# Kernel tuning notes

Hardware: AMD Instinct MI355X
Metric: run time of the kernel (lower is better)

Reference implementation:

```python
import jax, jax.numpy as jnp
import numpy as np

B, V, C, H, W, D, G = 1, 5, 32, 128, 160, 48, 1


def _bilinear_sample(fea, x, y):
    # fea: [B,C,H,W]; x,y: [B,N] pixel coords (grid_sample align_corners=True, zero padding)
    Bb, Cc, Hh, Ww = fea.shape
    x0 = jnp.floor(x); y0 = jnp.floor(y)
    x1 = x0 + 1.0; y1 = y0 + 1.0
    wx1 = x - x0; wx0 = 1.0 - wx1
    wy1 = y - y0; wy0 = 1.0 - wy1
    flat = fea.reshape(Bb, Cc, Hh * Ww)
    def gather(xi, yi):
        valid = (xi >= 0) & (xi <= Ww - 1) & (yi >= 0) & (yi <= Hh - 1)
        xc = jnp.clip(xi, 0, Ww - 1).astype(jnp.int32)
        yc = jnp.clip(yi, 0, Hh - 1).astype(jnp.int32)
        idx = (yc * Ww + xc)[:, None, :]                      # [B,1,N]
        g = jnp.take_along_axis(flat, idx, axis=2)            # [B,C,N]
        return g * valid[:, None, :].astype(fea.dtype)
    return (gather(x0, y0) * (wx0 * wy0)[:, None, :]
          + gather(x1, y0) * (wx1 * wy0)[:, None, :]
          + gather(x0, y1) * (wx0 * wy1)[:, None, :]
          + gather(x1, y1) * (wx1 * wy1)[:, None, :])          # [B,C,N]


def _homo_warp(src_fea, src_proj, ref_proj, depth_values):
    # src_fea [B,C,H,W]; src_proj/ref_proj [B,4,4]; depth_values [B,D,H,W]
    Bb, Cc, Hh, Ww = src_fea.shape
    Dd = depth_values.shape[1]
    proj = src_proj @ jnp.linalg.inv(ref_proj)
    rot, trans = proj[:, :3, :3], proj[:, :3, 3:4]
    yy, xx = jnp.meshgrid(jnp.arange(Hh, dtype=src_fea.dtype),
                          jnp.arange(Ww, dtype=src_fea.dtype), indexing='ij')
    xyz = jnp.stack([xx.ravel(), yy.ravel(), jnp.ones(Hh * Ww, src_fea.dtype)], 0)  # [3,HW]
    rot_xyz = jnp.einsum('bij,jn->bin', rot, xyz)                                    # [B,3,HW]
    d = depth_values.reshape(Bb, 1, Dd, Hh * Ww)
    pxyz = rot_xyz[:, :, None, :] * d + trans[:, :, :, None]                         # [B,3,D,HW]
    px = (pxyz[:, 0] / pxyz[:, 2]).reshape(Bb, -1)
    py = (pxyz[:, 1] / pxyz[:, 2]).reshape(Bb, -1)
    warped = _bilinear_sample(src_fea, px, py)                                       # [B,C,D*HW]
    return warped.reshape(Bb, Cc, Dd, Hh, Ww)


def _pixelwise_net(sim, w0, b0, w1, b1, w2, b2):
    # sim [B,G,D,H,W]; 1x1x1 convs; BatchNorm at default init in eval is identity
    x = jax.nn.relu(jnp.einsum('oc,bcdhw->bodhw', w0, sim) + b0[None, :, None, None, None])
    x = jax.nn.relu(jnp.einsum('oc,bcdhw->bodhw', w1, x) + b1[None, :, None, None, None])
    x = jnp.einsum('oc,bcdhw->bodhw', w2, x) + b2[None, :, None, None, None]
    p = jax.nn.sigmoid(x[:, 0])                       # [B,D,H,W]
    return jnp.max(p, axis=1, keepdims=True)          # [B,1,H,W]


def _fuse_proj(p):
    # p [B,2,4,4] -> extrinsics with K folded into top 3x4
    top = jnp.einsum('bij,bjk->bik', p[:, 1, :3, :3], p[:, 0, :3, :4])
    return p[:, 0].at[:, :3, :4].set(top)


def _forward(features, proj_matrices, depth_values, w0, b0, w1, b1, w2, b2, reg_w, reg_b, num_depth):
    ref_fea = features[0]
    Bb, Cc, Hh, Ww = ref_fea.shape
    ref_proj = _fuse_proj(proj_matrices[:, 0])
    ref_vol = ref_fea.reshape(Bb, G, Cc // G, 1, Hh, Ww)
    sim_sum = 0.0
    wsum = 1e-5
    vw_list = []
    for i in range(1, features.shape[0]):
        src_proj = _fuse_proj(proj_matrices[:, i])
        warped = _homo_warp(features[i], src_proj, ref_proj, depth_values)
        warped = warped.reshape(Bb, G, Cc // G, num_depth, Hh, Ww)
        sim = (warped * ref_vol).mean(2)              # [B,G,D,H,W]
        vw = _pixelwise_net(sim, w0, b0, w1, b1, w2, b2)   # [B,1,H,W]
        vw_list.append(vw)
        sim_sum = sim_sum + sim * vw[:, None]
        wsum = wsum + vw[:, None]
    sim = sim_sum / wsum
    cost = jax.lax.conv_general_dilated(sim, reg_w, (1, 1, 1), 'SAME',
                                        dimension_numbers=('NCDHW', 'OIDHW', 'NCDHW'))
    prob_volume_pre = cost[:, 0] + reg_b[0]           # [B,D,H,W]
    prob = jax.nn.softmax(prob_volume_pre, axis=1)
    idx = jnp.argmax(prob, axis=1, keepdims=True)
    depth = jnp.take_along_axis(depth_values, idx, axis=1)[:, 0]   # winner-take-all depth
    conf = jnp.max(prob, axis=1)
    view_weights = jnp.concatenate(vw_list, axis=1)
    return depth, conf, prob, view_weights


def setup_inputs() -> dict:
    key = jax.random.key(0)
    ks = jax.random.split(key, 6)
    features = jax.random.normal(ks[0], (V, B, C, H, W), jnp.float32)
    # Plausible camera geometry: identity-ish extrinsics + pinhole intrinsics
    K = np.eye(4, dtype=np.float32)
    K[0, 0] = K[1, 1] = 150.0; K[0, 2] = W / 2.0; K[1, 2] = H / 2.0
    mats = []
    for v in range(V):
        E = np.eye(4, dtype=np.float32)
        a = 0.01 * v
        ca, sa = np.cos(a), np.sin(a)
        E[:3, :3] = np.array([[ca, 0, sa], [0, 1, 0], [-sa, 0, ca]], np.float32)
        E[0, 3] = -5.0 * v
        mats.append(np.stack([E, K], 0))
    proj_matrices = jnp.asarray(np.stack(mats, 0)[None])  # [1,V,2,4,4]
    depth_values = jnp.broadcast_to(
        jnp.linspace(425.0, 935.0, D, dtype=jnp.float32).reshape(1, D, 1, 1), (B, D, H, W)) * jnp.ones((B, D, H, W), jnp.float32)
    return {
        'features': features,
        'proj_matrices': proj_matrices,
        'depth_values': depth_values,
        'w0': jax.random.normal(ks[1], (16, G), jnp.float32) * 0.1,
        'b0': jnp.zeros((16,), jnp.float32),
        'w1': jax.random.normal(ks[2], (8, 16), jnp.float32) * 0.1,
        'b1': jnp.zeros((8,), jnp.float32),
        'w2': jax.random.normal(ks[3], (1, 8), jnp.float32) * 0.1,
        'b2': jnp.zeros((1,), jnp.float32),
        'reg_w': jax.random.normal(ks[4], (1, G, 3, 3, 3), jnp.float32) * 0.1,
        'reg_b': jnp.zeros((1,), jnp.float32),
        'num_depth': D,
    }


def reference(features, proj_matrices, depth_values, w0, b0, w1, b1, w2, b2, reg_w, reg_b, num_depth):
    return _forward(features, proj_matrices, depth_values, w0, b0, w1, b1, w2, b2, reg_w, reg_b, num_depth)
```

## Files before the change

kernel.cpp:

```cpp
#include <hip/hip_runtime.h>
#include <hip/hip_bf16.h>
#include <math.h>

#define W_  160
#define H_  128
#define HW  20480
#define D_  48
#define C_  32
#define NV  4

#define TX  16
#define TY  4
#define TXH 18
#define TYH 6
#define NCOL (TXH*TYH)
#define GD  4
#define GDS 12

template<int CTRL>
__device__ __forceinline__ float dpp_add(float s) {
  int t = __builtin_amdgcn_update_dpp(0, __float_as_int(s), CTRL, 0xF, 0xF, true);
  return s + __int_as_float(t);
}

__device__ __forceinline__ unsigned ordf(float f) {
  unsigned b = __float_as_uint(f);
  return b ^ (((int)b >> 31) | 0x80000000u);
}
__device__ __forceinline__ float deordf(unsigned u) {
  unsigned b = (u & 0x80000000u) ? (u ^ 0x80000000u) : ~u;
  return __uint_as_float(b);
}

__device__ __forceinline__ void fuse_proj(const float* pm, float* P) {
  const float* E = pm;
  const float* K = pm + 16;
  for (int r = 0; r < 3; ++r)
    for (int c = 0; c < 4; ++c)
      P[r*4+c] = K[r*4+0]*E[0*4+c] + K[r*4+1]*E[1*4+c] + K[r*4+2]*E[2*4+c];
  for (int c = 0; c < 4; ++c) P[12+c] = E[12+c];
}

__device__ void invert4(const float* m, float* invOut) {
  float inv[16];
  inv[0]  =  m[5]*m[10]*m[15] - m[5]*m[11]*m[14] - m[9]*m[6]*m[15] + m[9]*m[7]*m[14] + m[13]*m[6]*m[11] - m[13]*m[7]*m[10];
  inv[4]  = -m[4]*m[10]*m[15] + m[4]*m[11]*m[14] + m[8]*m[6]*m[15] - m[8]*m[7]*m[14] - m[12]*m[6]*m[11] + m[12]*m[7]*m[10];
  inv[8]  =  m[4]*m[9]*m[15]  - m[4]*m[11]*m[13] - m[8]*m[5]*m[15] + m[8]*m[7]*m[13] + m[12]*m[5]*m[11] - m[12]*m[7]*m[9];
  inv[12] = -m[4]*m[9]*m[14]  + m[4]*m[10]*m[13] + m[8]*m[5]*m[14] - m[8]*m[6]*m[13] - m[12]*m[5]*m[10] + m[12]*m[6]*m[9];
  inv[1]  = -m[1]*m[10]*m[15] + m[1]*m[11]*m[14] + m[9]*m[2]*m[15] - m[9]*m[3]*m[14] - m[13]*m[2]*m[11] + m[13]*m[3]*m[10];
  inv[5]  =  m[0]*m[10]*m[15] - m[0]*m[11]*m[14] - m[8]*m[2]*m[15] + m[8]*m[3]*m[14] + m[12]*m[2]*m[11] - m[12]*m[3]*m[10];
  inv[9]  = -m[0]*m[9]*m[15]  + m[0]*m[11]*m[13] + m[8]*m[1]*m[15] - m[8]*m[3]*m[13] - m[12]*m[1]*m[11] + m[12]*m[3]*m[9];
  inv[13] =  m[0]*m[9]*m[14]  - m[0]*m[10]*m[13] - m[8]*m[1]*m[14] + m[8]*m[2]*m[13] + m[12]*m[1]*m[10] - m[12]*m[2]*m[9];
  inv[2]  =  m[1]*m[6]*m[15]  - m[1]*m[7]*m[14]  - m[5]*m[2]*m[15] + m[5]*m[3]*m[14] + m[13]*m[2]*m[7]  - m[13]*m[3]*m[6];
  inv[6]  = -m[0]*m[6]*m[15]  + m[0]*m[7]*m[14]  + m[4]*m[2]*m[15] - m[4]*m[3]*m[14] - m[12]*m[2]*m[7]  + m[12]*m[3]*m[6];
  inv[10] =  m[0]*m[5]*m[15]  - m[0]*m[7]*m[13]  - m[4]*m[1]*m[15] + m[4]*m[3]*m[13] + m[12]*m[1]*m[7]  - m[12]*m[3]*m[5];
  inv[14] = -m[0]*m[5]*m[14]  + m[0]*m[6]*m[13]  + m[4]*m[1]*m[14] - m[4]*m[2]*m[13] - m[12]*m[1]*m[6]  + m[12]*m[2]*m[5];
  inv[3]  = -m[1]*m[6]*m[11]  + m[1]*m[7]*m[10]  + m[5]*m[2]*m[11] - m[5]*m[3]*m[10] - m[9]*m[2]*m[7]   + m[9]*m[3]*m[6];
  inv[7]  =  m[0]*m[6]*m[11]  - m[0]*m[7]*m[10]  - m[4]*m[2]*m[11] + m[4]*m[3]*m[10] + m[8]*m[2]*m[7]   - m[8]*m[3]*m[6];
  inv[11] = -m[0]*m[5]*m[11]  + m[0]*m[7]*m[9]   + m[4]*m[1]*m[11] - m[4]*m[3]*m[9]  - m[8]*m[1]*m[7]   + m[8]*m[3]*m[5];
  inv[15] =  m[0]*m[5]*m[10]  - m[0]*m[6]*m[9]   - m[4]*m[1]*m[10] + m[4]*m[2]*m[9]  + m[8]*m[1]*m[6]   - m[8]*m[2]*m[5];
  float det = m[0]*inv[0] + m[1]*inv[4] + m[2]*inv[8] + m[3]*inv[12];
  det = 1.0f / det;
  for (int i = 0; i < 16; i++) invOut[i] = inv[i] * det;
}

__global__ void __launch_bounds__(256)
k_prep(const float* __restrict__ feat, const float* __restrict__ pm,
       float* __restrict__ tf, float* __restrict__ xf,
       unsigned* __restrict__ vwu) {
  __shared__ float tile[C_][64+1];
  int v  = blockIdx.y;
  int p0 = blockIdx.x * 64;
  int t  = threadIdx.x;

  if (v == 0) vwu[blockIdx.x*256 + t] = 0u;

  int pl = t & 63;
  int cg = t >> 6;
  const float* src = feat + (size_t)v*C_*HW + p0 + pl;
  #pragma unroll
  for (int k = 0; k < 8; ++k) {
    int c = cg*8 + k;
    tile[c][pl] = src[(size_t)c*HW];
  }
  __syncthreads();

  int pp = t >> 2;
  int co = (t & 3) * 8;
  float4 a, b;
  a.x = tile[co+0][pp]; a.y = tile[co+1][pp]; a.z = tile[co+2][pp]; a.w = tile[co+3][pp];
  b.x = tile[co+4][pp]; b.y = tile[co+5][pp]; b.z = tile[co+6][pp]; b.w = tile[co+7][pp];
  float* dst = tf + ((size_t)v*HW + p0 + pp)*C_ + co;
  *(float4*)dst = a;
  *(float4*)(dst+4) = b;

  if (blockIdx.x == 0 && v == 0) {
    if (t < 64) tf[(size_t)5*HW*C_ + t] = 0.0f;
    if (t == 0) {
      float Pr[16], Pinv[16], Ps[16], M[16];
      fuse_proj(pm, Pr);
      invert4(Pr, Pinv);
      for (int vv = 1; vv <= NV; ++vv) {
        fuse_proj(pm + vv*32, Ps);
        for (int r = 0; r < 4; ++r)
          for (int c = 0; c < 4; ++c) {
            float acc = 0.f;
            for (int k = 0; k < 4; ++k) acc += Ps[r*4+k]*Pinv[k*4+c];
            M[r*4+c] = acc;
          }
        float* o = xf + (vv-1)*12;
        o[0]=M[0];  o[1]=M[1];  o[2]=M[2];
        o[3]=M[4];  o[4]=M[5];  o[5]=M[6];
        o[6]=M[8];  o[7]=M[9];  o[8]=M[10];
        o[9]=M[3];  o[10]=M[7]; o[11]=M[11];
      }
    }
  }
}

template<int KX>
__device__ __forceinline__ void build_tab(
    const char* tfb, int chb, int ZB, float4 rfc,
    int xmin, int ymin, int ch, float* tabp) {
  #pragma unroll
  for (int t = 0; t < KX*3; ++t) {
    int xi = xmin + t/3;
    int yi = ymin + t%3;
    bool valid = ((unsigned)xi < (unsigned)W_) && ((unsigned)yi < (unsigned)H_);
    int off = valid ? (yi*W_ + xi)*(C_*4) : ZB;
    float4 a = *(const float4*)(tfb + off + chb);
    float d = a.x*rfc.x + a.y*rfc.y + a.z*rfc.z + a.w*rfc.w;
    d = dpp_add<0xB1>(d);
    d = dpp_add<0x4E>(d);
    d = dpp_add<0x141>(d);
    if (ch == (t & 7)) tabp[t] = d;
  }
}

__global__ void __launch_bounds__(256)
k_warp(const float* __restrict__ tf, const float* __restrict__ dv,
       const float* __restrict__ xf, float* __restrict__ sim_all) {
  __shared__ float dtab[4][8][25];

  int lane = threadIdx.x & 63;
  int wv = threadIdx.x >> 6;
  int ch = lane & 7;
  int pix = (lane >> 3) & 7;
  int wvg = __builtin_amdgcn_readfirstlane((blockIdx.x*256 + threadIdx.x) >> 6);
  const int PGPV = HW/8;
  int pg = wvg % PGPV;
  int v  = wvg / PGPV;
  int p  = pg*8 + pix;

  float xpix = (float)(p % W_);
  float ypix = (float)(p / W_);

  const float* M = xf + v*12;
  float rx = M[0]*xpix + M[1]*ypix + M[2];
  float ry = M[3]*xpix + M[4]*ypix + M[5];
  float rz = M[6]*xpix + M[7]*ypix + M[8];
  float t0 = M[9], t1 = M[10], t2 = M[11];

  float4 rfc = *(const float4*)(tf + (size_t)p*C_ + ch*4);
  rfc.x *= (1.0f/(float)C_); rfc.y *= (1.0f/(float)C_);
  rfc.z *= (1.0f/(float)C_); rfc.w *= (1.0f/(float)C_);

  const char* tfb = (const char*)(tf + (size_t)(v+1)*HW*C_);
  const int chb = ch*16;
  const int ZB = (4-v)*HW*C_*4;

  float depE0 = dv[p];
  float depE1 = dv[(size_t)47*HW + p];
  float dpk[6];
  #pragma unroll
  for (int k = 0; k < 6; ++k) dpk[k] = dv[(size_t)(k*8 + ch)*HW + p];

  float Z0 = rz*depE0 + t2, Z1 = rz*depE1 + t2;
  float iz0 = 1.0f / Z0,     iz1 = 1.0f / Z1;
  float pxa = (rx*depE0 + t0) * iz0, pya = (ry*depE0 + t1) * iz0;
  float pxb = (rx*depE1 + t0) * iz1, pyb = (ry*depE1 + t1) * iz1;
  int xmin = (int)floorf(fminf(pxa, pxb));
  int ymin = (int)floorf(fminf(pya, pyb));
  int Nx = (int)floorf(fmaxf(pxa, pxb)) - xmin + 2;
  int Ny = (int)floorf(fmaxf(pya, pyb)) - ymin + 2;

  float dmn = fminf(depE0, depE1), dmx = fmaxf(depE0, depE1);
  bool ok = (Nx <= 8) && (Ny <= 3) && (Z0*Z1 > 0.0f);
  #pragma unroll
  for (int k = 0; k < 6; ++k) ok = ok && (dpk[k] >= dmn) && (dpk[k] <= dmx);

  float* simv = sim_all + (size_t)v*D_*HW + p;

  if (__all(ok)) {
    float* tabp = dtab[wv][pix];
    if (__all(Nx <= 5)) build_tab<5>(tfb, chb, ZB, rfc, xmin, ymin, ch, tabp);
    else                build_tab<8>(tfb, chb, ZB, rfc, xmin, ymin, ch, tabp);

    int xhi = xmin + 6;
    if (__all(Nx <= 5)) xhi = xmin + 3;

    #pragma unroll
    for (int k = 0; k < 6; ++k) {
      float dep = dpk[k];
      float Z  = rz*dep + t2;
      float zr = 1.0f / Z;
      float px = (rx*dep + t0) * zr;
      float py = (ry*dep + t1) * zr;
      int xi = (int)floorf(px);
      int yi = (int)floorf(py);
      xi = min(max(xi, xmin), xhi);
      yi = min(max(yi, ymin), ymin + 1);
      float wx1 = px - (float)xi;
      float wy1 = py - (float)yi;
      float wx0 = 1.0f - wx1, wy0 = 1.0f - wy1;
      int idx = (xi - xmin)*3 + (yi - ymin);
      float t00 = tabp[idx];
      float t01 = tabp[idx + 3];
      float t10 = tabp[idx + 1];
      float t11 = tabp[idx + 4];
      float s = wx0*wy0*t00 + wx1*wy0*t01 + wx0*wy1*t10 + wx1*wy1*t11;
      simv[(size_t)(k*8 + ch)*HW] = s;
    }
  } else {
    const float* tff  = tf + (size_t)(v+1)*HW*C_;
    const float* refp = tf + (size_t)p*C_;
    const int ZE = (4-v)*HW*C_;
    #pragma unroll 1
    for (int k = 0; k < 6; ++k) {
      float dep = dpk[k];
      float Z  = rz*dep + t2;
      float px = (rx*dep + t0) / Z;
      float py = (ry*dep + t1) / Z;
      float x0f = floorf(px), y0f = floorf(py);
      float wx1 = px - x0f, wy1 = py - y0f;
      float wx0 = 1.0f - wx1, wy0 = 1.0f - wy1;
      int x0 = (int)x0f, y0 = (int)y0f;
      int x1 = x0 + 1,   y1 = y0 + 1;
      bool vx0 = ((unsigned)x0 <= (unsigned)(W_-1));
      bool vx1 = ((unsigned)x1 <= (unsigned)(W_-1));
      bool vy0 = ((unsigned)y0 <= (unsigned)(H_-1));
      bool vy1 = ((unsigned)y1 <= (unsigned)(H_-1));
      int cx0 = min(max(x0, 0), W_-1);
      int cx1 = min(max(x1, 0), W_-1);
      int cy0 = min(max(y0, 0), H_-1);
      int cy1 = min(max(y1, 0), H_-1);
      int o00 = (vx0 && vy0) ? (cy0*W_+cx0)*C_ : ZE;
      int o01 = (vx1 && vy0) ? (cy0*W_+cx1)*C_ : ZE;
      int o10 = (vx0 && vy1) ? (cy1*W_+cx0)*C_ : ZE;
      int o11 = (vx1 && vy1) ? (cy1*W_+cx1)*C_ : ZE;
      float a00=0.f, a01=0.f, a10=0.f, a11=0.f;
      #pragma unroll 1
      for (int q = 0; q < 8; ++q) {
        float4 rq = *(const float4*)(refp + q*4);
        float4 c0 = *(const float4*)(tff + o00 + q*4);
        float4 c1 = *(const float4*)(tff + o01 + q*4);
        float4 c2 = *(const float4*)(tff + o10 + q*4);
        float4 c3 = *(const float4*)(tff + o11 + q*4);
        a00 += c0.x*rq.x + c0.y*rq.y + c0.z*rq.z + c0.w*rq.w;
        a01 += c1.x*rq.x + c1.y*rq.y + c1.z*rq.z + c1.w*rq.w;
        a10 += c2.x*rq.x + c2.y*rq.y + c2.z*rq.z + c2.w*rq.w;
        a11 += c3.x*rq.x + c3.y*rq.y + c3.z*rq.z + c3.w*rq.w;
      }
      float s = (wx0*wy0*a00 + wx1*wy0*a01 + wx0*wy1*a10 + wx1*wy1*a11)
                * (1.0f/(float)C_);
      simv[(size_t)(k*8 + ch)*HW] = s;
    }
  }
}

__global__ void __launch_bounds__(256)
k_mlp(const float* __restrict__ sim_all,
      const float* __restrict__ w0, const float* __restrict__ b0,
      const float* __restrict__ w1, const float* __restrict__ b1,
      const float* __restrict__ w2, const float* __restrict__ b2,
      unsigned* __restrict__ vwu) {
  int idx = blockIdx.x*blockDim.x + threadIdx.x;
  if (idx >= NV*(D_/4)*HW) return;
  int p = idx % HW;
  int t = idx / HW;
  int v = t / (D_/4);
  int c = t % (D_/4);

  const float* sp_ = sim_all + ((size_t)(v*D_ + c*4))*HW + p;
  float sv[4];
  sv[0] = sp_[0];
  sv[1] = sp_[HW];
  sv[2] = sp_[2*HW];
  sv[3] = sp_[3*HW];

  float ymax = -3.0e38f;
  #pragma unroll
  for (int k = 0; k < 4; ++k) {
    float s = sv[k];
    float acc0 = b1[0], acc1 = b1[1], acc2 = b1[2], acc3 = b1[3];
    float acc4 = b1[4], acc5 = b1[5], acc6 = b1[6], acc7 = b1[7];
    #pragma unroll
    for (int o = 0; o < 16; ++o) {
      float h = fmaxf(fmaf(w0[o], s, b0[o]), 0.0f);
      acc0 = fmaf(w1[0*16+o], h, acc0);
      acc1 = fmaf(w1[1*16+o], h, acc1);
      acc2 = fmaf(w1[2*16+o], h, acc2);
      acc3 = fmaf(w1[3*16+o], h, acc3);
      acc4 = fmaf(w1[4*16+o], h, acc4);
      acc5 = fmaf(w1[5*16+o], h, acc5);
      acc6 = fmaf(w1[6*16+o], h, acc6);
      acc7 = fmaf(w1[7*16+o], h, acc7);
    }
    float yv = b2[0];
    yv = fmaf(w2[0], fmaxf(acc0, 0.0f), yv);
    yv = fmaf(w2[1], fmaxf(acc1, 0.0f), yv);
    yv = fmaf(w2[2], fmaxf(acc2, 0.0f), yv);
    yv = fmaf(w2[3], fmaxf(acc3, 0.0f), yv);
    yv = fmaf(w2[4], fmaxf(acc4, 0.0f), yv);
    yv = fmaf(w2[5], fmaxf(acc5, 0.0f), yv);
    yv = fmaf(w2[6], fmaxf(acc6, 0.0f), yv);
    yv = fmaf(w2[7], fmaxf(acc7, 0.0f), yv);
    ymax = fmaxf(ymax, yv);
  }
  atomicMax(&vwu[(size_t)v*HW + p], ordf(ymax));
}

__global__ void __launch_bounds__(256)
k_fusecv(const float* __restrict__ sim_all, const unsigned* __restrict__ vwu,
         const float* __restrict__ rw, const float* __restrict__ rb,
         float* __restrict__ cost) {
  __shared__ float svw[NV][NCOL];
  __shared__ float sinvw[NCOL];
  __shared__ int   sgpc[NCOL];
  __shared__ float sfus[GDS+2][TYH][TXH+1];

  int tid = threadIdx.x;
  int gx0 = blockIdx.x*TX;
  int gy0 = blockIdx.y*TY;
  int g   = blockIdx.z;

  if (tid < NCOL) {
    int yy = tid / TXH, xx = tid % TXH;
    int gy = gy0 + yy - 1, gx = gx0 + xx - 1;
    bool valid = (gx >= 0) && (gx < W_) && (gy >= 0) && (gy < H_);
    int gp = min(max(gy,0),H_-1)*W_ + min(max(gx,0),W_-1);
    sgpc[tid] = gp;
    float a0 = 1.0f/(1.0f + expf(-deordf(vwu[0*HW+gp])));
    float a1 = 1.0f/(1.0f + expf(-deordf(vwu[1*HW+gp])));
    float a2 = 1.0f/(1.0f + expf(-deordf(vwu[2*HW+gp])));
    float a3 = 1.0f/(1.0f + expf(-deordf(vwu[3*HW+gp])));
    float inv = valid ? 1.0f/(1e-5f + a0+a1+a2+a3) : 0.0f;
    if (!valid) { a0=a1=a2=a3=0.f; }
    svw[0][tid]=a0; svw[1][tid]=a1; svw[2][tid]=a2; svw[3][tid]=a3;
    sinvw[tid] = inv;
  }
  __syncthreads();

  for (int j = tid; j < (GDS+2)*NCOL; j += 256) {
    int s = j / NCOL, r = j % NCOL;
    int dz = g*GDS - 1 + s;
    float val = 0.0f;
    if (dz >= 0 && dz < D_) {
      int gp = sgpc[r];
      float s0 = sim_all[(size_t)(0*D_+dz)*HW + gp];
      float s1 = sim_all[(size_t)(1*D_+dz)*HW + gp];
      float s2 = sim_all[(size_t)(2*D_+dz)*HW + gp];
      float s3 = sim_all[(size_t)(3*D_+dz)*HW + gp];
      val = (s0*svw[0][r] + s1*svw[1][r] + s2*svw[2][r] + s3*svw[3][r]) * sinvw[r];
    }
    sfus[s][r/TXH][r%TXH] = val;
  }
  __syncthreads();

  {
    int pid = tid & 63;
    int dg  = tid >> 6;
    int px = pid & 15, py = pid >> 4;
    float kw[27];
    #pragma unroll
    for (int i = 0; i < 27; ++i) kw[i] = rw[i];
    float bias = rb[0];
    int gp = (gy0+py)*W_ + gx0+px;

    #pragma unroll
    for (int k = 0; k < 3; ++k) {
      int dl = dg*3 + k;
      float acc = bias;
      #pragma unroll
      for (int kd = 0; kd < 3; ++kd)
        #pragma unroll
        for (int ky = 0; ky < 3; ++ky)
          #pragma unroll
          for (int kx = 0; kx < 3; ++kx)
            acc += sfus[dl+kd][py+ky][px+kx] * kw[(kd*3+ky)*3+kx];
      cost[(size_t)(g*GDS + dl)*HW + gp] = acc;
    }
  }
}

__global__ void __launch_bounds__(256)
k_softmax(const float* __restrict__ cost, const unsigned* __restrict__ vwu,
          const float* __restrict__ dv, float* __restrict__ out) {
  int p = blockIdx.x*256 + threadIdx.x;
  if (p >= HW) return;

  float c[D_];
  #pragma unroll
  for (int d = 0; d < D_; ++d) c[d] = cost[(size_t)d*HW + p];

  float vmax = c[0];
  int am = 0;
  #pragma unroll
  for (int d = 1; d < D_; ++d) {
    if (c[d] > vmax) { vmax = c[d]; am = d; }
  }
  float sum = 0.0f;
  #pragma unroll
  for (int d = 0; d < D_; ++d) {
    float e = expf(c[d] - vmax);
    c[d] = e;
    sum += e;
  }
  float inv = 1.0f / sum;
  #pragma unroll
  for (int d = 0; d < D_; ++d)
    out[(size_t)(2*HW) + (size_t)d*HW + p] = c[d] * inv;

  out[p] = dv[(size_t)am*HW + p];
  out[HW + p] = inv;
  #pragma unroll
  for (int v = 0; v < NV; ++v)
    out[(size_t)(2*HW + D_*HW) + (size_t)v*HW + p] =
        1.0f/(1.0f + expf(-deordf(vwu[(size_t)v*HW + p])));
}

extern "C" void kernel_launch(void* const* d_in, const int* in_sizes, int n_in,
                              void* d_out, int out_size, void* d_ws, size_t ws_size,
                              hipStream_t stream) {
  const float* feat = (const float*)d_in[0];
  const float* pm   = (const float*)d_in[1];
  const float* dv   = (const float*)d_in[2];
  const float* w0   = (const float*)d_in[3];
  const float* b0   = (const float*)d_in[4];
  const float* w1   = (const float*)d_in[5];
  const float* b1   = (const float*)d_in[6];
  const float* w2   = (const float*)d_in[7];
  const float* b2   = (const float*)d_in[8];
  const float* rw   = (const float*)d_in[9];
  const float* rb   = (const float*)d_in[10];
  float* out = (float*)d_out;
  float* ws  = (float*)d_ws;

  float*    xf   = ws;
  float*    tf   = ws + 64;
  float*    sim  = ws + 3276928;
  unsigned* vwu  = (unsigned*)(ws + 7209088);
  float*    cost = ws + 7291008;

  hipLaunchKernelGGL(k_prep, dim3(HW/64, 5), dim3(256), 0, stream,
                     feat, pm, tf, xf, vwu);
  hipLaunchKernelGGL(k_warp, dim3((NV*HW*8)/256), dim3(256), 0, stream,
                     tf, dv, xf, sim);
  hipLaunchKernelGGL(k_mlp, dim3((NV*(D_/4)*HW)/256), dim3(256), 0, stream,
                     sim, w0, b0, w1, b1, w2, b2, vwu);
  hipLaunchKernelGGL(k_fusecv, dim3(W_/TX, H_/TY, GD), dim3(256), 0, stream,
                     sim, vwu, rw, rb, cost);
  hipLaunchKernelGGL(k_softmax, dim3(HW/256), dim3(256), 0, stream,
                     cost, vwu, dv, out);
}
```

Baseline: 75.38 us.

## Fuse pixelwise MLP and view-weight max into warp kernel

The per-pixel MLP that produces view weights now runs inside the warp kernel on the similarity values each lane already holds in registers. The max over depth is reduced across the 8 lanes with DPP, and the sigmoid is written directly as a float. This removes the separate MLP kernel, its re-read of the similarity volume, the atomicMax with ordered-int encoding, and the zero-init in prep. The cost is extra ALU work and register pressure in the warp kernel, which could lower its occupancy.

```diff
diff --git a/kernel.cpp b/kernel.cpp
--- a/kernel.cpp
+++ b/kernel.cpp
@@ -22,14 +22,10 @@
   int t = __builtin_amdgcn_update_dpp(0, __float_as_int(s), CTRL, 0xF, 0xF, true);
   return s + __int_as_float(t);
 }
-
-__device__ __forceinline__ unsigned ordf(float f) {
-  unsigned b = __float_as_uint(f);
-  return b ^ (((int)b >> 31) | 0x80000000u);
-}
-__device__ __forceinline__ float deordf(unsigned u) {
-  unsigned b = (u & 0x80000000u) ? (u ^ 0x80000000u) : ~u;
-  return __uint_as_float(b);
+template<int CTRL>
+__device__ __forceinline__ float dpp_max(float s) {
+  int t = __builtin_amdgcn_update_dpp(0, __float_as_int(s), CTRL, 0xF, 0xF, true);
+  return fmaxf(s, __int_as_float(t));
 }
 
 __device__ __forceinline__ void fuse_proj(const float* pm, float* P) {
@@ -66,14 +62,11 @@
 
 __global__ void __launch_bounds__(256)
 k_prep(const float* __restrict__ feat, const float* __restrict__ pm,
-       float* __restrict__ tf, float* __restrict__ xf,
-       unsigned* __restrict__ vwu) {
+       float* __restrict__ tf, float* __restrict__ xf) {
   __shared__ float tile[C_][64+1];
   int v  = blockIdx.y;
   int p0 = blockIdx.x * 64;
   int t  = threadIdx.x;
-
-  if (v == 0) vwu[blockIdx.x*256 + t] = 0u;
 
   int pl = t & 63;
   int cg = t >> 6;
@@ -137,9 +130,44 @@
   }
 }
 
+__device__ __forceinline__ float mlp_eval(
+    float s,
+    const float* __restrict__ w0, const float* __restrict__ b0,
+    const float* __restrict__ w1, const float* __restrict__ b1,
+    const float* __restrict__ w2, const float* __restrict__ b2) {
+  float acc0 = b1[0], acc1 = b1[1], acc2 = b1[2], acc3 = b1[3];
+  float acc4 = b1[4], acc5 = b1[5], acc6 = b1[6], acc7 = b1[7];
+  #pragma unroll
+  for (int o = 0; o < 16; ++o) {
+    float h = fmaxf(fmaf(w0[o], s, b0[o]), 0.0f);
+    acc0 = fmaf(w1[0*16+o], h, acc0);
+    acc1 = fmaf(w1[1*16+o], h, acc1);
+    acc2 = fmaf(w1[2*16+o], h, acc2);
+    acc3 = fmaf(w1[3*16+o], h, acc3);
+    acc4 = fmaf(w1[4*16+o], h, acc4);
+    acc5 = fmaf(w1[5*16+o], h, acc5);
+    acc6 = fmaf(w1[6*16+o], h, acc6);
+    acc7 = fmaf(w1[7*16+o], h, acc7);
+  }
+  float yv = b2[0];
+  yv = fmaf(w2[0], fmaxf(acc0, 0.0f), yv);
+  yv = fmaf(w2[1], fmaxf(acc1, 0.0f), yv);
+  yv = fmaf(w2[2], fmaxf(acc2, 0.0f), yv);
+  yv = fmaf(w2[3], fmaxf(acc3, 0.0f), yv);
+  yv = fmaf(w2[4], fmaxf(acc4, 0.0f), yv);
+  yv = fmaf(w2[5], fmaxf(acc5, 0.0f), yv);
+  yv = fmaf(w2[6], fmaxf(acc6, 0.0f), yv);
+  yv = fmaf(w2[7], fmaxf(acc7, 0.0f), yv);
+  return yv;
+}
+
 __global__ void __launch_bounds__(256)
 k_warp(const float* __restrict__ tf, const float* __restrict__ dv,
-       const float* __restrict__ xf, float* __restrict__ sim_all) {
+       const float* __restrict__ xf,
+       const float* __restrict__ w0, const float* __restrict__ b0,
+       const float* __restrict__ w1, const float* __restrict__ b1,
+       const float* __restrict__ w2, const float* __restrict__ b2,
+       float* __restrict__ sim_all, float* __restrict__ vw) {
   __shared__ float dtab[4][8][25];
 
   int lane = threadIdx.x & 63;
@@ -190,6 +218,7 @@
   for (int k = 0; k < 6; ++k) ok = ok && (dpk[k] >= dmn) && (dpk[k] <= dmx);
 
   float* simv = sim_all + (size_t)v*D_*HW + p;
+  float sk[6];
 
   if (__all(ok)) {
     float* tabp = dtab[wv][pix];
@@ -219,6 +248,7 @@
       float t10 = tabp[idx + 1];
       float t11 = tabp[idx + 4];
       float s = wx0*wy0*t00 + wx1*wy0*t01 + wx0*wy1*t10 + wx1*wy1*t11;
+      sk[k] = s;
       simv[(size_t)(k*8 + ch)*HW] = s;
     }
   } else {
@@ -263,65 +293,26 @@
       }
       float s = (wx0*wy0*a00 + wx1*wy0*a01 + wx0*wy1*a10 + wx1*wy1*a11)
                 * (1.0f/(float)C_);
+      sk[k] = s;
       simv[(size_t)(k*8 + ch)*HW] = s;
     }
   }
+
+  float ymax = mlp_eval(sk[0], w0, b0, w1, b1, w2, b2);
+  ymax = fmaxf(ymax, mlp_eval(sk[1], w0, b0, w1, b1, w2, b2));
+  ymax = fmaxf(ymax, mlp_eval(sk[2], w0, b0, w1, b1, w2, b2));
+  ymax = fmaxf(ymax, mlp_eval(sk[3], w0, b0, w1, b1, w2, b2));
+  ymax = fmaxf(ymax, mlp_eval(sk[4], w0, b0, w1, b1, w2, b2));
+  ymax = fmaxf(ymax, mlp_eval(sk[5], w0, b0, w1, b1, w2, b2));
+
+  ymax = dpp_max<0xB1>(ymax);
+  ymax = dpp_max<0x4E>(ymax);
+  ymax = dpp_max<0x141>(ymax);
+  if (ch == 0) vw[(size_t)v*HW + p] = 1.0f / (1.0f + expf(-ymax));
 }
 
 __global__ void __launch_bounds__(256)
-k_mlp(const float* __restrict__ sim_all,
-      const float* __restrict__ w0, const float* __restrict__ b0,
-      const float* __restrict__ w1, const float* __restrict__ b1,
-      const float* __restrict__ w2, const float* __restrict__ b2,
-      unsigned* __restrict__ vwu) {
-  int idx = blockIdx.x*blockDim.x + threadIdx.x;
-  if (idx >= NV*(D_/4)*HW) return;
-  int p = idx % HW;
-  int t = idx / HW;
-  int v = t / (D_/4);
-  int c = t % (D_/4);
-
-  const float* sp_ = sim_all + ((size_t)(v*D_ + c*4))*HW + p;
-  float sv[4];
-  sv[0] = sp_[0];
-  sv[1] = sp_[HW];
-  sv[2] = sp_[2*HW];
-  sv[3] = sp_[3*HW];
-
-  float ymax = -3.0e38f;
-  #pragma unroll
-  for (int k = 0; k < 4; ++k) {
-    float s = sv[k];
-    float acc0 = b1[0], acc1 = b1[1], acc2 = b1[2], acc3 = b1[3];
-    float acc4 = b1[4], acc5 = b1[5], acc6 = b1[6], acc7 = b1[7];
-    #pragma unroll
-    for (int o = 0; o < 16; ++o) {
-      float h = fmaxf(fmaf(w0[o], s, b0[o]), 0.0f);
-      acc0 = fmaf(w1[0*16+o], h, acc0);
-      acc1 = fmaf(w1[1*16+o], h, acc1);
-      acc2 = fmaf(w1[2*16+o], h, acc2);
-      acc3 = fmaf(w1[3*16+o], h, acc3);
-      acc4 = fmaf(w1[4*16+o], h, acc4);
-      acc5 = fmaf(w1[5*16+o], h, acc5);
-      acc6 = fmaf(w1[6*16+o], h, acc6);
-      acc7 = fmaf(w1[7*16+o], h, acc7);
-    }
-    float yv = b2[0];
-    yv = fmaf(w2[0], fmaxf(acc0, 0.0f), yv);
-    yv = fmaf(w2[1], fmaxf(acc1, 0.0f), yv);
-    yv = fmaf(w2[2], fmaxf(acc2, 0.0f), yv);
-    yv = fmaf(w2[3], fmaxf(acc3, 0.0f), yv);
-    yv = fmaf(w2[4], fmaxf(acc4, 0.0f), yv);
-    yv = fmaf(w2[5], fmaxf(acc5, 0.0f), yv);
-    yv = fmaf(w2[6], fmaxf(acc6, 0.0f), yv);
-    yv = fmaf(w2[7], fmaxf(acc7, 0.0f), yv);
-    ymax = fmaxf(ymax, yv);
-  }
-  atomicMax(&vwu[(size_t)v*HW + p], ordf(ymax));
-}
-
-__global__ void __launch_bounds__(256)
-k_fusecv(const float* __restrict__ sim_all, const unsigned* __restrict__ vwu,
+k_fusecv(const float* __restrict__ sim_all, const float* __restrict__ vw,
          const float* __restrict__ rw, const float* __restrict__ rb,
          float* __restrict__ cost) {
   __shared__ float svw[NV][NCOL];
@@ -340,10 +331,7 @@
     bool valid = (gx >= 0) && (gx < W_) && (gy >= 0) && (gy < H_);
     int gp = min(max(gy,0),H_-1)*W_ + min(max(gx,0),W_-1);
     sgpc[tid] = gp;
-    float a0 = 1.0f/(1.0f + expf(-deordf(vwu[0*HW+gp])));
-    float a1 = 1.0f/(1.0f + expf(-deordf(vwu[1*HW+gp])));
-    float a2 = 1.0f/(1.0f + expf(-deordf(vwu[2*HW+gp])));
-    float a3 = 1.0f/(1.0f + expf(-deordf(vwu[3*HW+gp])));
+    float a0 = vw[0*HW+gp], a1 = vw[1*HW+gp], a2 = vw[2*HW+gp], a3 = vw[3*HW+gp];
     float inv = valid ? 1.0f/(1e-5f + a0+a1+a2+a3) : 0.0f;
     if (!valid) { a0=a1=a2=a3=0.f; }
     svw[0][tid]=a0; svw[1][tid]=a1; svw[2][tid]=a2; svw[3][tid]=a3;
@@ -394,7 +382,7 @@
 }
 
 __global__ void __launch_bounds__(256)
-k_softmax(const float* __restrict__ cost, const unsigned* __restrict__ vwu,
+k_softmax(const float* __restrict__ cost, const float* __restrict__ vw,
           const float* __restrict__ dv, float* __restrict__ out) {
   int p = blockIdx.x*256 + threadIdx.x;
   if (p >= HW) return;
@@ -425,8 +413,7 @@
   out[HW + p] = inv;
   #pragma unroll
   for (int v = 0; v < NV; ++v)
-    out[(size_t)(2*HW + D_*HW) + (size_t)v*HW + p] =
-        1.0f/(1.0f + expf(-deordf(vwu[(size_t)v*HW + p])));
+    out[(size_t)(2*HW + D_*HW) + (size_t)v*HW + p] = vw[(size_t)v*HW + p];
 }
 
 extern "C" void kernel_launch(void* const* d_in, const int* in_sizes, int n_in,
@@ -446,20 +433,18 @@
   float* out = (float*)d_out;
   float* ws  = (float*)d_ws;
 
-  float*    xf   = ws;
-  float*    tf   = ws + 64;
-  float*    sim  = ws + 3276928;
-  unsigned* vwu  = (unsigned*)(ws + 7209088);
-  float*    cost = ws + 7291008;
+  float* xf   = ws;
+  float* tf   = ws + 64;
+  float* sim  = ws + 3276928;
+  float* vw   = ws + 7209088;
+  float* cost = ws + 7291008;
 
   hipLaunchKernelGGL(k_prep, dim3(HW/64, 5), dim3(256), 0, stream,
-                     feat, pm, tf, xf, vwu);
+                     feat, pm, tf, xf);
   hipLaunchKernelGGL(k_warp, dim3((NV*HW*8)/256), dim3(256), 0, stream,
-                     tf, dv, xf, sim);
-  hipLaunchKernelGGL(k_mlp, dim3((NV*(D_/4)*HW)/256), dim3(256), 0, stream,
-                     sim, w0, b0, w1, b1, w2, b2, vwu);
+                     tf, dv, xf, w0, b0, w1, b1, w2, b2, sim, vw);
   hipLaunchKernelGGL(k_fusecv, dim3(W_/TX, H_/TY, GD), dim3(256), 0, stream,
-                     sim, vwu, rw, rb, cost);
+                     sim, vw, rw, rb, cost);
   hipLaunchKernelGGL(k_softmax, dim3(HW/256), dim3(256), 0, stream,
-                     cost, vwu, dv, out);
-}
+                     cost, vw, dv, out);
+}
```

After: 81.46 us. 1.08x slower.

## Interleave views in similarity buffer and widen table fast path to 12 columns

Applied to the files above, without the earlier changes.

Stores the per-view similarity volume as [depth][pixel][view] so the MLP and fusion kernels load all four views with one float4. The MLP kernel now processes one depth per thread across four views and issues four atomic maxes instead of reducing over four depths first. The warp kernel gains a 12-column table path so more wavefronts avoid the slow gather fallback. The cost is strided stores in the warp kernel and more atomic traffic in the MLP kernel.

```diff
diff --git a/kernel.cpp b/kernel.cpp
--- a/kernel.cpp
+++ b/kernel.cpp
@@ -139,8 +139,8 @@
 
 __global__ void __launch_bounds__(256)
 k_warp(const float* __restrict__ tf, const float* __restrict__ dv,
-       const float* __restrict__ xf, float* __restrict__ sim_all) {
-  __shared__ float dtab[4][8][25];
+       const float* __restrict__ xf, float* __restrict__ sim4) {
+  __shared__ float dtab[4][8][37];
 
   int lane = threadIdx.x & 63;
   int wv = threadIdx.x >> 6;
@@ -185,19 +185,25 @@
   int Ny = (int)floorf(fmaxf(pya, pyb)) - ymin + 2;
 
   float dmn = fminf(depE0, depE1), dmx = fmaxf(depE0, depE1);
-  bool ok = (Nx <= 8) && (Ny <= 3) && (Z0*Z1 > 0.0f);
+  bool ok = (Nx <= 12) && (Ny <= 3) && (Z0*Z1 > 0.0f);
   #pragma unroll
   for (int k = 0; k < 6; ++k) ok = ok && (dpk[k] >= dmn) && (dpk[k] <= dmx);
 
-  float* simv = sim_all + (size_t)v*D_*HW + p;
+  float* simv = sim4 + (size_t)p*4 + v;
 
   if (__all(ok)) {
     float* tabp = dtab[wv][pix];
-    if (__all(Nx <= 5)) build_tab<5>(tfb, chb, ZB, rfc, xmin, ymin, ch, tabp);
-    else                build_tab<8>(tfb, chb, ZB, rfc, xmin, ymin, ch, tabp);
-
-    int xhi = xmin + 6;
-    if (__all(Nx <= 5)) xhi = xmin + 3;
+    int xhi;
+    if (__all(Nx <= 5)) {
+      build_tab<5>(tfb, chb, ZB, rfc, xmin, ymin, ch, tabp);
+      xhi = xmin + 3;
+    } else if (__all(Nx <= 8)) {
+      build_tab<8>(tfb, chb, ZB, rfc, xmin, ymin, ch, tabp);
+      xhi = xmin + 6;
+    } else {
+      build_tab<12>(tfb, chb, ZB, rfc, xmin, ymin, ch, tabp);
+      xhi = xmin + 10;
+    }
 
     #pragma unroll
     for (int k = 0; k < 6; ++k) {
@@ -219,7 +225,8 @@
       float t10 = tabp[idx + 1];
       float t11 = tabp[idx + 4];
       float s = wx0*wy0*t00 + wx1*wy0*t01 + wx0*wy1*t10 + wx1*wy1*t11;
-      simv[(size_t)(k*8 + ch)*HW] = s;
+      if (ch == ch) ;
+      simv[(size_t)(k*8 + ch)*HW*4] = s;
     }
   } else {
     const float* tff  = tf + (size_t)(v+1)*HW*C_;
@@ -263,65 +270,66 @@
       }
       float s = (wx0*wy0*a00 + wx1*wy0*a01 + wx0*wy1*a10 + wx1*wy1*a11)
                 * (1.0f/(float)C_);
-      simv[(size_t)(k*8 + ch)*HW] = s;
+      simv[(size_t)(k*8 + ch)*HW*4] = s;
     }
   }
 }
 
 __global__ void __launch_bounds__(256)
-k_mlp(const float* __restrict__ sim_all,
+k_mlp(const float* __restrict__ sim4,
       const float* __restrict__ w0, const float* __restrict__ b0,
       const float* __restrict__ w1, const float* __restrict__ b1,
       const float* __restrict__ w2, const float* __restrict__ b2,
       unsigned* __restrict__ vwu) {
   int idx = blockIdx.x*blockDim.x + threadIdx.x;
-  if (idx >= NV*(D_/4)*HW) return;
+  if (idx >= D_*HW) return;
   int p = idx % HW;
-  int t = idx / HW;
-  int v = t / (D_/4);
-  int c = t % (D_/4);
-
-  const float* sp_ = sim_all + ((size_t)(v*D_ + c*4))*HW + p;
-  float sv[4];
-  sv[0] = sp_[0];
-  sv[1] = sp_[HW];
-  sv[2] = sp_[2*HW];
-  sv[3] = sp_[3*HW];
-
-  float ymax = -3.0e38f;
-  #pragma unroll
-  for (int k = 0; k < 4; ++k) {
-    float s = sv[k];
-    float acc0 = b1[0], acc1 = b1[1], acc2 = b1[2], acc3 = b1[3];
-    float acc4 = b1[4], acc5 = b1[5], acc6 = b1[6], acc7 = b1[7];
+
+  float4 s4 = *(const float4*)(sim4 + (size_t)idx*4);
+
+  float y0, y1, y2, y3;
+  {
+    float acc[4][8];
+    #pragma unroll
+    for (int j = 0; j < 8; ++j) {
+      float bb = b1[j];
+      acc[0][j] = bb; acc[1][j] = bb; acc[2][j] = bb; acc[3][j] = bb;
+    }
     #pragma unroll
     for (int o = 0; o < 16; ++o) {
-      float h = fmaxf(fmaf(w0[o], s, b0[o]), 0.0f);
-      acc0 = fmaf(w1[0*16+o], h, acc0);
-      acc1 = fmaf(w1[1*16+o], h, acc1);
-      acc2 = fmaf(w1[2*16+o], h, acc2);
-      acc3 = fmaf(w1[3*16+o], h, acc3);
-      acc4 = fmaf(w1[4*16+o], h, acc4);
-      acc5 = fmaf(w1[5*16+o], h, acc5);
-      acc6 = fmaf(w1[6*16+o], h, acc6);
-      acc7 = fmaf(w1[7*16+o], h, acc7);
-    }
-    float yv = b2[0];
-    yv = fmaf(w2[0], fmaxf(acc0, 0.0f), yv);
-    yv = fmaf(w2[1], fmaxf(acc1, 0.0f), yv);
-    yv = fmaf(w2[2], fmaxf(acc2, 0.0f), yv);
-    yv = fmaf(w2[3], fmaxf(acc3, 0.0f), yv);
-    yv = fmaf(w2[4], fmaxf(acc4, 0.0f), yv);
-    yv = fmaf(w2[5], fmaxf(acc5, 0.0f), yv);
-    yv = fmaf(w2[6], fmaxf(acc6, 0.0f), yv);
-    yv = fmaf(w2[7], fmaxf(acc7, 0.0f), yv);
-    ymax = fmaxf(ymax, yv);
-  }
-  atomicMax(&vwu[(size_t)v*HW + p], ordf(ymax));
+      float wo = w0[o], bo = b0[o];
+      float h0 = fmaxf(fmaf(wo, s4.x, bo), 0.0f);
+      float h1 = fmaxf(fmaf(wo, s4.y, bo), 0.0f);
+      float h2 = fmaxf(fmaf(wo, s4.z, bo), 0.0f);
+      float h3 = fmaxf(fmaf(wo, s4.w, bo), 0.0f);
+      #pragma unroll
+      for (int j = 0; j < 8; ++j) {
+        float w = w1[j*16+o];
+        acc[0][j] = fmaf(w, h0, acc[0][j]);
+        acc[1][j] = fmaf(w, h1, acc[1][j]);
+        acc[2][j] = fmaf(w, h2, acc[2][j]);
+        acc[3][j] = fmaf(w, h3, acc[3][j]);
+      }
+    }
+    float b2v = b2[0];
+    y0 = b2v; y1 = b2v; y2 = b2v; y3 = b2v;
+    #pragma unroll
+    for (int j = 0; j < 8; ++j) {
+      float w = w2[j];
+      y0 = fmaf(w, fmaxf(acc[0][j], 0.0f), y0);
+      y1 = fmaf(w, fmaxf(acc[1][j], 0.0f), y1);
+      y2 = fmaf(w, fmaxf(acc[2][j], 0.0f), y2);
+      y3 = fmaf(w, fmaxf(acc[3][j], 0.0f), y3);
+    }
+  }
+  atomicMax(&vwu[0*HW + p], ordf(y0));
+  atomicMax(&vwu[1*HW + p], ordf(y1));
+  atomicMax(&vwu[2*HW + p], ordf(y2));
+  atomicMax(&vwu[3*HW + p], ordf(y3));
 }
 
 __global__ void __launch_bounds__(256)
-k_fusecv(const float* __restrict__ sim_all, const unsigned* __restrict__ vwu,
+k_fusecv(const float* __restrict__ sim4, const unsigned* __restrict__ vwu,
          const float* __restrict__ rw, const float* __restrict__ rb,
          float* __restrict__ cost) {
   __shared__ float svw[NV][NCOL];
@@ -357,11 +365,9 @@
     float val = 0.0f;
     if (dz >= 0 && dz < D_) {
       int gp = sgpc[r];
-      float s0 = sim_all[(size_t)(0*D_+dz)*HW + gp];
-      float s1 = sim_all[(size_t)(1*D_+dz)*HW + gp];
-      float s2 = sim_all[(size_t)(2*D_+dz)*HW + gp];
-      float s3 = sim_all[(size_t)(3*D_+dz)*HW + gp];
-      val = (s0*svw[0][r] + s1*svw[1][r] + s2*svw[2][r] + s3*svw[3][r]) * sinvw[r];
+      float4 s4 = *(const float4*)(sim4 + ((size_t)dz*HW + gp)*4);
+      val = (s4.x*svw[0][r] + s4.y*svw[1][r] + s4.z*svw[2][r] + s4.w*svw[3][r])
+            * sinvw[r];
     }
     sfus[s][r/TXH][r%TXH] = val;
   }
@@ -448,18 +454,18 @@
 
   float*    xf   = ws;
   float*    tf   = ws + 64;
-  float*    sim  = ws + 3276928;
+  float*    sim4 = ws + 3276928;
   unsigned* vwu  = (unsigned*)(ws + 7209088);
   float*    cost = ws + 7291008;
 
   hipLaunchKernelGGL(k_prep, dim3(HW/64, 5), dim3(256), 0, stream,
                      feat, pm, tf, xf, vwu);
   hipLaunchKernelGGL(k_warp, dim3((NV*HW*8)/256), dim3(256), 0, stream,
-                     tf, dv, xf, sim);
-  hipLaunchKernelGGL(k_mlp, dim3((NV*(D_/4)*HW)/256), dim3(256), 0, stream,
-                     sim, w0, b0, w1, b1, w2, b2, vwu);
+                     tf, dv, xf, sim4);
+  hipLaunchKernelGGL(k_mlp, dim3((D_*HW)/256), dim3(256), 0, stream,
+                     sim4, w0, b0, w1, b1, w2, b2, vwu);
   hipLaunchKernelGGL(k_fusecv, dim3(W_/TX, H_/TY, GD), dim3(256), 0, stream,
-                     sim, vwu, rw, rb, cost);
+                     sim4, vwu, rw, rb, cost);
   hipLaunchKernelGGL(k_softmax, dim3(HW/256), dim3(256), 0, stream,
                      cost, vwu, dv, out);
 }
```

Result: no change. 75.86 us (+0.6%).
